# Kernel tuning notes

Hardware: AMD Instinct MI355X
Metric: run time of the kernel (lower is better)

## Reference

```python
import jax, jax.numpy as jnp
import numpy as np

L, D, H, DH, DF = 4, 512, 8, 64, 2048
B, S = 4, 2048
EPS = 1e-6  # fast-transformers causal-linear eps


def _ln(x, g, b, eps=1e-5):
    mu = jnp.mean(x, axis=-1, keepdims=True)
    var = jnp.var(x, axis=-1, keepdims=True)
    return (x - mu) * jax.lax.rsqrt(var + eps) * g + b


def _causal_linear(Q, K, V):
    # Q, K, V: [B, S, H, DH]; O(N) linear-attention recurrence over S
    Qs = jnp.moveaxis(Q, 1, 0)
    Ks = jnp.moveaxis(K, 1, 0)
    Vs = jnp.moveaxis(V, 1, 0)
    b = Q.shape[0]
    kv0 = jnp.zeros((b, H, DH, DH), Q.dtype)  # running sum of k v^T
    z0 = jnp.zeros((b, H, DH), Q.dtype)       # running sum of k

    def step(carry, qkv):
        kv, z = carry
        q, k, v = qkv  # each [B, H, DH]
        kv = kv + k[..., :, None] * v[..., None, :]
        z = z + k
        num = jnp.einsum('bhd,bhdm->bhm', q, kv)
        den = jnp.einsum('bhd,bhd->bh', q, z) + EPS
        return (kv, z), num / den[..., None]

    _, out = jax.lax.scan(step, (kv0, z0), (Qs, Ks, Vs))
    return jnp.moveaxis(out, 0, 1)  # [B, S, H, DH]


def _layer(x, p):
    Wq, bq, Wk, bk, Wv, bv, Wo, bo, W1, b1, W2, b2, g1, be1, g2, be2 = p
    b, s, _ = x.shape
    q = (x @ Wq + bq).reshape(b, s, H, DH)
    k = (x @ Wk + bk).reshape(b, s, H, DH)
    v = (x @ Wv + bv).reshape(b, s, H, DH)
    Qf = jax.nn.elu(q) + 1.0  # feature map phi(x) = elu(x) + 1
    Kf = jax.nn.elu(k) + 1.0
    a = _causal_linear(Qf, Kf, v).reshape(b, s, D)
    x = x + (a @ Wo + bo)            # residual (dropout=0)
    x = _ln(x, g1, be1)              # post-norm
    y = jax.nn.gelu(x @ W1 + b1, approximate=False) @ W2 + b2
    return _ln(x + y, g2, be2)


def _encoder(h, params, gf, bef):
    def body(x, p):
        return _layer(x, p), None
    x, _ = jax.lax.scan(body, h, params)
    return _ln(x, gf, bef)  # final LayerNorm from builder


def setup_inputs() -> dict:
    key = jax.random.key(0)
    ks = jax.random.split(key, 8)

    def w(k, shape, fan_in):
        return jax.random.normal(k, shape, jnp.float32) * (fan_in ** -0.5)

    return {
        'h': jax.random.normal(ks[0], (B, S, D), jnp.float32),
        'Wq': w(ks[1], (L, D, D), D), 'bq': jnp.zeros((L, D), jnp.float32),
        'Wk': w(ks[2], (L, D, D), D), 'bk': jnp.zeros((L, D), jnp.float32),
        'Wv': w(ks[3], (L, D, D), D), 'bv': jnp.zeros((L, D), jnp.float32),
        'Wo': w(ks[4], (L, D, D), D), 'bo': jnp.zeros((L, D), jnp.float32),
        'W1': w(ks[5], (L, D, DF), D), 'b1': jnp.zeros((L, DF), jnp.float32),
        'W2': w(ks[6], (L, DF, D), DF), 'b2': jnp.zeros((L, D), jnp.float32),
        'g1': jnp.ones((L, D), jnp.float32), 'be1': jnp.zeros((L, D), jnp.float32),
        'g2': jnp.ones((L, D), jnp.float32), 'be2': jnp.zeros((L, D), jnp.float32),
        'gf': jnp.ones((D,), jnp.float32), 'bef': jnp.zeros((D,), jnp.float32),
    }


def reference(h, Wq, bq, Wk, bk, Wv, bv, Wo, bo, W1, b1, W2, b2,
              g1, be1, g2, be2, gf, bef):
    params = (Wq, bq, Wk, bk, Wv, bv, Wo, bo, W1, b1, W2, b2, g1, be1, g2, be2)
    return _encoder(h, params, gf, bef)
```

## Files before the change

### kernel.cpp

```cpp
#include <hip/hip_runtime.h>
#include <hip/hip_bf16.h>
#include <math.h>

#define LAYERS 4
#define DMODEL 512
#define NH 8
#define DH 64
#define DFF 2048
#define NB 4
#define S_LEN 2048
#define MROWS 8192
#define CHUNK 64
#define NCHUNK 32
#define ATT_EPS 1e-6f
#define LN_EPS 1e-5f
#define SEGSTRIDE (MROWS * DMODEL)

typedef __attribute__((ext_vector_type(8))) short short8v;
typedef __attribute__((ext_vector_type(4))) float f32x4;

__device__ __forceinline__ float b2f(unsigned short u) {
    union { float f; unsigned u; } c; c.u = ((unsigned)u) << 16; return c.f;
}
__device__ __forceinline__ unsigned short f2b(float f) {
    union { float f; unsigned u; } c; c.f = f;
    unsigned r = c.u + 0x7FFFu + ((c.u >> 16) & 1u);
    return (unsigned short)(r >> 16);
}
__device__ __forceinline__ void gload16(const void* g, void* l) {
    __builtin_amdgcn_global_load_lds(
        (const __attribute__((address_space(1))) void*)g,
        (__attribute__((address_space(3))) void*)l, 16, 0, 0);
}
__device__ __forceinline__ float elu1f(float v) {
    return (v > 0.f) ? (v + 1.f) : __expf(v);
}
__device__ __forceinline__ float geluf(float v) {
    float u = 0.7978845608028654f * v * (1.f + 0.044715f * v * v);
    float th = 1.f - 2.f / (1.f + __expf(2.f * u));
    return 0.5f * v * (1.f + th);
}

template <int ACT, bool RESID, bool ATOMIC, bool WU, bool WBF16, int KSPLIT>
__global__ __launch_bounds__(512, 4) void gemm8(
    const unsigned short* __restrict__ A,
    const unsigned short* __restrict__ WT,
    const float* __restrict__ b0, const float* __restrict__ b1,
    const float* __restrict__ b2,
    const unsigned short* __restrict__ Xres,
    float* __restrict__ U, unsigned short* __restrict__ Cbf,
    int M, int N, int K)
{
    __shared__ short S[2][16384];

    const int t = threadIdx.x;
    const int m0 = blockIdx.x * 128, n0 = blockIdx.y * 128;
    const int kz = (KSPLIT > 1) ? blockIdx.z : 0;
    const int Kc = K / KSPLIT;
    const int kbeg = kz * Kc;
    const int lane = t & 63, wid = t >> 6;
    const int wm = (wid >> 2) * 64;
    const int wn = (wid & 3) * 32;
    const int fr = lane & 15, kg = lane >> 4;

    const unsigned short* gsrc[4];
    int ldso[4];
#pragma unroll
    for (int r = 0; r < 4; ++r) {
        const int u = (r & 1) ? (t + 512) : t;
        const bool isA = (r < 2);
        const int row = u >> 3, sp = u & 7, sl = sp ^ (row & 7);
        gsrc[r] = (isA ? A + (size_t)(m0 + row) * K
                       : WT + (size_t)(n0 + row) * K) + kbeg + sl * 8;
        ldso[r] = (isA ? 0 : 8192) + u * 8;
    }

    int aoff[2][4], boff[2][2];
#pragma unroll
    for (int h = 0; h < 2; ++h) {
#pragma unroll
        for (int m = 0; m < 4; ++m) {
            const int R = wm + m * 16 + fr;
            aoff[h][m] = R * 64 + (((h * 4 + kg) ^ (R & 7)) * 8);
        }
#pragma unroll
        for (int n = 0; n < 2; ++n) {
            const int R = wn + n * 16 + fr;
            boff[h][n] = 8192 + R * 64 + (((h * 4 + kg) ^ (R & 7)) * 8);
        }
    }

    f32x4 acc[4][2];
#pragma unroll
    for (int m = 0; m < 4; ++m)
#pragma unroll
        for (int n = 0; n < 2; ++n) acc[m][n] = (f32x4){0.f, 0.f, 0.f, 0.f};

#define STAGE(b, kt) do { _Pragma("unroll")                                  \
    for (int r = 0; r < 4; ++r)                                              \
        gload16(gsrc[r] + (size_t)(kt) * 64, &S[b][ldso[r]]); } while (0)

    const int NT = Kc >> 6;
    STAGE(0, 0);

    for (int td = 0; td < NT; ++td) {
        const int b = td & 1;
        if (td + 1 < NT) {
            STAGE(b ^ 1, td + 1);
            __builtin_amdgcn_sched_barrier(0);
            asm volatile("s_waitcnt vmcnt(4)");
        } else {
            __builtin_amdgcn_sched_barrier(0);
            asm volatile("s_waitcnt vmcnt(0)");
        }
        __builtin_amdgcn_sched_barrier(0);
        __builtin_amdgcn_s_barrier();
        __builtin_amdgcn_sched_barrier(0);

        short8v a0[4], b0f[2], a1[4], b1f[2];
#pragma unroll
        for (int m = 0; m < 4; ++m) a0[m] = *(const short8v*)&S[b][aoff[0][m]];
#pragma unroll
        for (int n = 0; n < 2; ++n) b0f[n] = *(const short8v*)&S[b][boff[0][n]];
#pragma unroll
        for (int m = 0; m < 4; ++m) a1[m] = *(const short8v*)&S[b][aoff[1][m]];
#pragma unroll
        for (int n = 0; n < 2; ++n) b1f[n] = *(const short8v*)&S[b][boff[1][n]];

        asm volatile("s_waitcnt lgkmcnt(6)");
        __builtin_amdgcn_sched_barrier(0);
        __builtin_amdgcn_s_setprio(1);
#pragma unroll
        for (int m = 0; m < 4; ++m)
#pragma unroll
            for (int n = 0; n < 2; ++n)
                acc[m][n] = __builtin_amdgcn_mfma_f32_16x16x32_bf16(
                    a0[m], b0f[n], acc[m][n], 0, 0, 0);
        __builtin_amdgcn_s_setprio(0);

        asm volatile("s_waitcnt lgkmcnt(0)");
        __builtin_amdgcn_sched_barrier(0);
        __builtin_amdgcn_s_setprio(1);
#pragma unroll
        for (int m = 0; m < 4; ++m)
#pragma unroll
            for (int n = 0; n < 2; ++n)
                acc[m][n] = __builtin_amdgcn_mfma_f32_16x16x32_bf16(
                    a1[m], b1f[n], acc[m][n], 0, 0, 0);
        __builtin_amdgcn_s_setprio(0);

        __builtin_amdgcn_sched_barrier(0);
        __builtin_amdgcn_s_barrier();
    }
#undef STAGE

    const int seg = (ACT == 3) ? (n0 >> 9) : 0;
    const float* bias = (ACT == 3) ? (seg == 0 ? b0 : (seg == 1 ? b1 : b2)) : b0;
    float bv[2];
#pragma unroll
    for (int n = 0; n < 2; ++n) {
        const int col = n0 + wn + n * 16 + fr;
        bv[n] = bias[(ACT == 3) ? (col - seg * 512) : col];
    }
    if (KSPLIT > 1 && kz != 0) { bv[0] = 0.f; bv[1] = 0.f; }

#pragma unroll
    for (int m = 0; m < 4; ++m)
#pragma unroll
        for (int n = 0; n < 2; ++n)
#pragma unroll
            for (int j = 0; j < 4; ++j) {
                const int row = m0 + wm + m * 16 + (lane >> 4) * 4 + j;
                const int col = n0 + wn + n * 16 + fr;
                float v = acc[m][n][j] + bv[n];
                if (RESID && kz == 0)
                    v += b2f(Xres[(size_t)row * 512 + col]);
                if (ACT == 1) v = elu1f(v);
                else if (ACT == 2) v = geluf(v);
                else if (ACT == 3) { if (seg < 2) v = elu1f(v); }
                if (ATOMIC) {
                    atomicAdd(&U[(size_t)row * N + col], v);
                } else if (WU) {
                    U[(size_t)row * N + col] = v;
                }
                if (WBF16) {
                    if (ACT == 3)
                        Cbf[(size_t)seg * SEGSTRIDE + (size_t)row * 512 + (col - seg * 512)] = f2b(v);
                    else
                        Cbf[(size_t)row * N + col] = f2b(v);
                }
            }
}

__global__ __launch_bounds__(256) void transpose_to_bf16(
    const float* __restrict__ W, unsigned short* __restrict__ WT, int K, int N)
{
    __shared__ float tile[32][33];
    const int k0 = blockIdx.x * 32, n0 = blockIdx.y * 32;
    const int tx = threadIdx.x & 31, ty = threadIdx.x >> 5;
#pragma unroll
    for (int i = ty; i < 32; i += 8)
        tile[i][tx] = W[(size_t)(k0 + i) * N + n0 + tx];
    __syncthreads();
#pragma unroll
    for (int i = ty; i < 32; i += 8)
        WT[(size_t)(n0 + i) * K + k0 + tx] = f2b(tile[tx][i]);
}

__global__ __launch_bounds__(256) void cvt_in(
    const float* __restrict__ h, unsigned short* __restrict__ xb, int n)
{
    const int i = (blockIdx.x * 256 + threadIdx.x) * 8;
    if (i >= n) return;
    f32x4 a = *(const f32x4*)(h + i);
    f32x4 b = *(const f32x4*)(h + i + 4);
    short8v p;
    p[0] = f2b(a[0]); p[1] = f2b(a[1]); p[2] = f2b(a[2]); p[3] = f2b(a[3]);
    p[4] = f2b(b[0]); p[5] = f2b(b[1]); p[6] = f2b(b[2]); p[7] = f2b(b[3]);
    *(short8v*)(xb + i) = p;
}

__device__ __forceinline__ int swzo(int row, int sl) {
    return row * 64 + ((sl ^ (row & 7)) << 3);
}

__global__ __launch_bounds__(256) void attn_stage1(
    const unsigned short* __restrict__ Kf, const unsigned short* __restrict__ Vf,
    unsigned short* __restrict__ KVp, float* __restrict__ zp)
{
    const int c = blockIdx.x, hh = blockIdx.y, bb = blockIdx.z;
    const int t = threadIdx.x;
    const int lane = t & 63, w = t >> 6;
    const int fr = lane & 15, g = lane >> 4;

    __shared__ unsigned short KTs[64 * 72];
    __shared__ unsigned short VTs[64 * 72];

    const size_t rowbase = (size_t)(bb * S_LEN + c * CHUNK);
    const int colbase = hh * DH;

    {
        const int r = lane, cs = w * 16;
        const unsigned short* kp = Kf + (rowbase + r) * DMODEL + colbase + cs;
        const unsigned short* vp = Vf + (rowbase + r) * DMODEL + colbase + cs;
        short8v k0 = *(const short8v*)kp, k1 = *(const short8v*)(kp + 8);
        short8v v0 = *(const short8v*)vp, v1 = *(const short8v*)(vp + 8);
#pragma unroll
        for (int i = 0; i < 8; ++i) {
            KTs[(cs + i) * 72 + r]     = (unsigned short)k0[i];
            KTs[(cs + 8 + i) * 72 + r] = (unsigned short)k1[i];
            VTs[(cs + i) * 72 + r]     = (unsigned short)v0[i];
            VTs[(cs + 8 + i) * 72 + r] = (unsigned short)v1[i];
        }
    }
    __syncthreads();

    f32x4 cacc[4];
#pragma unroll
    for (int nf = 0; nf < 4; ++nf) cacc[nf] = (f32x4){0.f, 0.f, 0.f, 0.f};

    const short8v a0 = *(const short8v*)&VTs[(w * 16 + fr) * 72 + g * 8];
    const short8v a1 = *(const short8v*)&VTs[(w * 16 + fr) * 72 + (4 + g) * 8];
#pragma unroll
    for (int nf = 0; nf < 4; ++nf) {
        short8v bq0 = *(const short8v*)&KTs[(nf * 16 + fr) * 72 + g * 8];
        short8v bq1 = *(const short8v*)&KTs[(nf * 16 + fr) * 72 + (4 + g) * 8];
        cacc[nf] = __builtin_amdgcn_mfma_f32_16x16x32_bf16(a0, bq0, cacc[nf], 0, 0, 0);
        cacc[nf] = __builtin_amdgcn_mfma_f32_16x16x32_bf16(a1, bq1, cacc[nf], 0, 0, 0);
    }

    const size_t base = ((size_t)(bb * NH + hh) * NCHUNK + c) * (DH * DH);
#pragma unroll
    for (int nf = 0; nf < 4; ++nf)
#pragma unroll
        for (int reg = 0; reg < 4; ++reg) {
            const int e = w * 16 + g * 4 + reg;
            const int d = nf * 16 + fr;
            KVp[base + e * 64 + d] = f2b(cacc[nf][reg]);
        }

    if (t < 64) {
        float s = 0.f;
#pragma unroll
        for (int sl = 0; sl < 8; ++sl) {
            short8v kv = *(const short8v*)&KTs[t * 72 + sl * 8];
#pragma unroll
            for (int i = 0; i < 8; ++i) s += b2f((unsigned short)kv[i]);
        }
        zp[((size_t)(bb * NH + hh) * NCHUNK + c) * DH + t] = s;
    }
}

__global__ __launch_bounds__(256) void attn_stage2(
    const unsigned short* __restrict__ KVp, unsigned short* __restrict__ KVb,
    float* __restrict__ zp)
{
    const int bh = blockIdx.x;
    const int e = blockIdx.y * 256 + threadIdx.x;
    const size_t base = (size_t)bh * NCHUNK * (DH * DH) + e;
    float run = 0.f;
#pragma unroll 4
    for (int c = 0; c < NCHUNK; ++c) {
        const float tmp = b2f(KVp[base + (size_t)c * (DH * DH)]);
        KVb[base + (size_t)c * (DH * DH)] = f2b(run);
        run += tmp;
    }
    if (blockIdx.y == 0 && threadIdx.x < DH) {
        float rz = 0.f;
        const size_t zb = (size_t)bh * NCHUNK * DH + threadIdx.x;
#pragma unroll 4
        for (int c = 0; c < NCHUNK; ++c) {
            const float tmp = zp[zb + c * DH];
            zp[zb + c * DH] = rz;
            rz += tmp;
        }
    }
}

__global__ __launch_bounds__(256) void attn_stage3(
    const unsigned short* __restrict__ Qf, const unsigned short* __restrict__ Kf,
    const unsigned short* __restrict__ Vf, const unsigned short* __restrict__ KVb,
    const float* __restrict__ zp, unsigned short* __restrict__ Af)
{
    const int c = blockIdx.x, hh = blockIdx.y, bb = blockIdx.z;
    const int t = threadIdx.x;
    const int lane = t & 63, w = t >> 6;
    const int fr = lane & 15, g = lane >> 4;

    __shared__ unsigned short Qs[4096];
    __shared__ unsigned short Ks[4096];
    __shared__ unsigned short KVts[4096];
    __shared__ unsigned short VTs[64 * 72];
    __shared__ unsigned short Ps[64 * 72];
    __shared__ float zsh[DH];
    __shared__ float den_lds[64];

    const size_t rowbase = (size_t)(bb * S_LEN + c * CHUNK);
    const int colbase = hh * DH;
    const size_t kvbase = ((size_t)(bb * NH + hh) * NCHUNK + c) * (DH * DH);

#pragma unroll
    for (int iss = 0; iss < 2; ++iss) {
        const int u = iss * 256 + t, row = u >> 3, sl = u & 7;
        const int ssl = (sl ^ (row & 7)) * 8;
        gload16(Qf + (rowbase + row) * DMODEL + colbase + ssl, &Qs[(size_t)u * 8]);
        gload16(Kf + (rowbase + row) * DMODEL + colbase + ssl, &Ks[(size_t)u * 8]);
        gload16(KVb + kvbase + row * 64 + ssl, &KVts[(size_t)u * 8]);
    }
    {
        const int r = lane, cs = w * 16;
        const unsigned short* vp = Vf + (rowbase + r) * DMODEL + colbase + cs;
        short8v v0 = *(const short8v*)vp, v1 = *(const short8v*)(vp + 8);
#pragma unroll
        for (int i = 0; i < 8; ++i) {
            VTs[(cs + i) * 72 + r]     = (unsigned short)v0[i];
            VTs[(cs + 8 + i) * 72 + r] = (unsigned short)v1[i];
        }
    }
    if (t < DH) zsh[t] = zp[((size_t)(bb * NH + hh) * NCHUNK + c) * DH + t];
    __syncthreads();

    f32x4 c1[4];
#pragma unroll
    for (int mf = 0; mf < 4; ++mf) c1[mf] = (f32x4){0.f, 0.f, 0.f, 0.f};
    {
        const short8v bq0 = *(const short8v*)&Qs[swzo(w * 16 + fr, g)];
        const short8v bq1 = *(const short8v*)&Qs[swzo(w * 16 + fr, 4 + g)];
#pragma unroll
        for (int mf = 0; mf < 4; ++mf) {
            short8v ak0 = *(const short8v*)&Ks[swzo(mf * 16 + fr, g)];
            short8v ak1 = *(const short8v*)&Ks[swzo(mf * 16 + fr, 4 + g)];
            c1[mf] = __builtin_amdgcn_mfma_f32_16x16x32_bf16(ak0, bq0, c1[mf], 0, 0, 0);
            c1[mf] = __builtin_amdgcn_mfma_f32_16x16x32_bf16(ak1, bq1, c1[mf], 0, 0, 0);
        }
    }

    const int i_my = w * 16 + fr;
    float dint = 0.f;
#pragma unroll
    for (int mf = 0; mf < 4; ++mf)
#pragma unroll
        for (int reg = 0; reg < 4; ++reg) {
            const int j = mf * 16 + g * 4 + reg;
            const float v = (j <= i_my) ? c1[mf][reg] : 0.f;
            dint += v;
            Ps[i_my * 72 + j] = f2b(v);
        }
    dint += __shfl_xor(dint, 16);
    dint += __shfl_xor(dint, 32);

    float dpre = 0.f;
#pragma unroll
    for (int sl = 0; sl < 8; ++sl) {
        short8v qv = *(const short8v*)&Qs[swzo(i_my, sl)];
#pragma unroll
        for (int e = 0; e < 8; ++e) dpre += b2f((unsigned short)qv[e]) * zsh[sl * 8 + e];
    }
    if (g == 0) den_lds[i_my] = dpre + dint + ATT_EPS;

    f32x4 acc[4];
#pragma unroll
    for (int nf = 0; nf < 4; ++nf) acc[nf] = (f32x4){0.f, 0.f, 0.f, 0.f};
    {
        const short8v aq0 = *(const short8v*)&Qs[swzo(w * 16 + fr, g)];
        const short8v aq1 = *(const short8v*)&Qs[swzo(w * 16 + fr, 4 + g)];
#pragma unroll
        for (int nf = 0; nf < 4; ++nf) {
            short8v bkv0 = *(const short8v*)&KVts[swzo(nf * 16 + fr, g)];
            short8v bkv1 = *(const short8v*)&KVts[swzo(nf * 16 + fr, 4 + g)];
            acc[nf] = __builtin_amdgcn_mfma_f32_16x16x32_bf16(aq0, bkv0, acc[nf], 0, 0, 0);
            acc[nf] = __builtin_amdgcn_mfma_f32_16x16x32_bf16(aq1, bkv1, acc[nf], 0, 0, 0);
        }
        const short8v ap0 = *(const short8v*)&Ps[(w * 16 + fr) * 72 + g * 8];
        const short8v ap1 = *(const short8v*)&Ps[(w * 16 + fr) * 72 + (4 + g) * 8];
#pragma unroll
        for (int nf = 0; nf < 4; ++nf) {
            short8v bv0 = *(const short8v*)&VTs[(nf * 16 + fr) * 72 + g * 8];
            short8v bv1 = *(const short8v*)&VTs[(nf * 16 + fr) * 72 + (4 + g) * 8];
            acc[nf] = __builtin_amdgcn_mfma_f32_16x16x32_bf16(ap0, bv0, acc[nf], 0, 0, 0);
            acc[nf] = __builtin_amdgcn_mfma_f32_16x16x32_bf16(ap1, bv1, acc[nf], 0, 0, 0);
        }
    }

#pragma unroll
    for (int reg = 0; reg < 4; ++reg) {
        const int i = w * 16 + g * 4 + reg;
        const float inv = 1.f / den_lds[i];
        unsigned short* dst = Af + (rowbase + i) * DMODEL + colbase;
#pragma unroll
        for (int nf = 0; nf < 4; ++nf)
            dst[nf * 16 + fr] = f2b(acc[nf][reg] * inv);
    }
}

__global__ __launch_bounds__(256) void ln_u2x(float* __restrict__ U,
                                              const float* __restrict__ g,
                                              const float* __restrict__ b,
                                              unsigned short* __restrict__ Xb,
                                              int ZERO)
{
    const size_t row = blockIdx.x * 4 + (threadIdx.x >> 6);
    const int t = threadIdx.x & 63;
    float* ur = U + row * DMODEL;
    f32x4 x0 = *(const f32x4*)&ur[t * 4];
    f32x4 x1 = *(const f32x4*)&ur[256 + t * 4];

    float s  = x0[0] + x0[1] + x0[2] + x0[3] + x1[0] + x1[1] + x1[2] + x1[3];
    float sq = x0[0]*x0[0] + x0[1]*x0[1] + x0[2]*x0[2] + x0[3]*x0[3] +
               x1[0]*x1[0] + x1[1]*x1[1] + x1[2]*x1[2] + x1[3]*x1[3];
#pragma unroll
    for (int m = 1; m < 64; m <<= 1) {
        s  += __shfl_xor(s, m);
        sq += __shfl_xor(sq, m);
    }
    const float mu  = s * (1.f / DMODEL);
    const float var = sq * (1.f / DMODEL) - mu * mu;
    const float rr  = rsqrtf(var + LN_EPS);

    const int c0 = t * 4, c1 = 256 + t * 4;
    f32x4 g0 = *(const f32x4*)&g[c0], g1v = *(const f32x4*)&g[c1];
    f32x4 b0 = *(const f32x4*)&b[c0], b1v = *(const f32x4*)&b[c1];
    unsigned short* xb = Xb + row * DMODEL;
    ushort4 u0, u1;
    u0.x = f2b((x0[0] - mu) * rr * g0[0] + b0[0]);
    u0.y = f2b((x0[1] - mu) * rr * g0[1] + b0[1]);
    u0.z = f2b((x0[2] - mu) * rr * g0[2] + b0[2]);
    u0.w = f2b((x0[3] - mu) * rr * g0[3] + b0[3]);
    u1.x = f2b((x1[0] - mu) * rr * g1v[0] + b1v[0]);
    u1.y = f2b((x1[1] - mu) * rr * g1v[1] + b1v[1]);
    u1.z = f2b((x1[2] - mu) * rr * g1v[2] + b1v[2]);
    u1.w = f2b((x1[3] - mu) * rr * g1v[3] + b1v[3]);
    *(ushort4*)&xb[c0] = u0;
    *(ushort4*)&xb[c1] = u1;
    if (ZERO) {
        *(f32x4*)&ur[c0] = (f32x4){0.f, 0.f, 0.f, 0.f};
        *(f32x4*)&ur[c1] = (f32x4){0.f, 0.f, 0.f, 0.f};
    }
}

__global__ __launch_bounds__(256) void ln_final(const unsigned short* __restrict__ Xb,
                                                const float* __restrict__ g,
                                                const float* __restrict__ b,
                                                float* __restrict__ Out)
{
    const size_t row = blockIdx.x * 4 + (threadIdx.x >> 6);
    const int t = threadIdx.x & 63;
    const unsigned short* xr = Xb + row * DMODEL;
    short8v xv = *(const short8v*)&xr[t * 8];
    float x[8];
#pragma unroll
    for (int i = 0; i < 8; ++i) x[i] = b2f((unsigned short)xv[i]);

    float s = 0.f, sq = 0.f;
#pragma unroll
    for (int i = 0; i < 8; ++i) { s += x[i]; sq += x[i] * x[i]; }
#pragma unroll
    for (int m = 1; m < 64; m <<= 1) {
        s  += __shfl_xor(s, m);
        sq += __shfl_xor(sq, m);
    }
    const float mu  = s * (1.f / DMODEL);
    const float var = sq * (1.f / DMODEL) - mu * mu;
    const float rr  = rsqrtf(var + LN_EPS);

    float* orow = Out + row * DMODEL + t * 8;
    f32x4 o0, o1;
#pragma unroll
    for (int i = 0; i < 4; ++i) {
        o0[i] = (x[i] - mu) * rr * g[t * 8 + i] + b[t * 8 + i];
        o1[i] = (x[4 + i] - mu) * rr * g[t * 8 + 4 + i] + b[t * 8 + 4 + i];
    }
    *(f32x4*)orow = o0;
    *(f32x4*)(orow + 4) = o1;
}

extern "C" void kernel_launch(void* const* d_in, const int* in_sizes, int n_in,
                              void* d_out, int out_size, void* d_ws, size_t ws_size,
                              hipStream_t stream)
{
    const float* h   = (const float*)d_in[0];
    const float* Wq  = (const float*)d_in[1];
    const float* bq  = (const float*)d_in[2];
    const float* Wk  = (const float*)d_in[3];
    const float* bk  = (const float*)d_in[4];
    const float* Wv  = (const float*)d_in[5];
    const float* bv  = (const float*)d_in[6];
    const float* Wo  = (const float*)d_in[7];
    const float* bo  = (const float*)d_in[8];
    const float* W1  = (const float*)d_in[9];
    const float* b1  = (const float*)d_in[10];
    const float* W2  = (const float*)d_in[11];
    const float* b2  = (const float*)d_in[12];
    const float* g1  = (const float*)d_in[13];
    const float* be1 = (const float*)d_in[14];
    const float* g2  = (const float*)d_in[15];
    const float* be2 = (const float*)d_in[16];
    const float* gf  = (const float*)d_in[17];
    const float* bef = (const float*)d_in[18];

    char* ws = (char*)d_ws;
    const size_t MB = 1024 * 1024;
    unsigned short* x_bf = (unsigned short*)(ws);
    unsigned short* qkv  = (unsigned short*)(ws + 8 * MB);
    unsigned short* qb   = qkv;
    unsigned short* kb   = qkv + SEGSTRIDE;
    unsigned short* vb   = qkv + 2 * (size_t)SEGSTRIDE;
    unsigned short* ab   = (unsigned short*)(ws + 32 * MB);
    unsigned short* hid  = (unsigned short*)(ws + 8 * MB);
    unsigned short* KVp  = (unsigned short*)(ws + 40 * MB);
    unsigned short* KVb  = (unsigned short*)(ws + 48 * MB);
    float* U             = (float*)(ws + 40 * MB);
    float* zp            = (float*)(ws + 56 * MB);
    unsigned short* WTall = (unsigned short*)(ws + 57 * MB);

    const int M = MROWS, D = DMODEL, DF = DFF;
    const size_t LSTR = 3 * 1024 * 1024;

    cvt_in<<<dim3(M * D / (256 * 8)), 256, 0, stream>>>(h, x_bf, M * D);
    for (int l = 0; l < LAYERS; ++l) {
        unsigned short* WL = WTall + (size_t)l * LSTR;
        transpose_to_bf16<<<dim3(D / 32, D / 32), 256, 0, stream>>>(Wq + (size_t)l * D * D, WL, D, D);
        transpose_to_bf16<<<dim3(D / 32, D / 32), 256, 0, stream>>>(Wk + (size_t)l * D * D, WL + 262144, D, D);
        transpose_to_bf16<<<dim3(D / 32, D / 32), 256, 0, stream>>>(Wv + (size_t)l * D * D, WL + 524288, D, D);
        transpose_to_bf16<<<dim3(D / 32, D / 32), 256, 0, stream>>>(Wo + (size_t)l * D * D, WL + 786432, D, D);
        transpose_to_bf16<<<dim3(D / 32, DF / 32), 256, 0, stream>>>(W1 + (size_t)l * D * DF, WL + 1048576, D, DF);
        transpose_to_bf16<<<dim3(DF / 32, D / 32), 256, 0, stream>>>(W2 + (size_t)l * DF * D, WL + 2097152, DF, D);
    }

    for (int l = 0; l < LAYERS; ++l) {
        unsigned short* WL = WTall + (size_t)l * LSTR;
        const unsigned short* WqkvT = WL;
        const unsigned short* WoT   = WL + 786432;
        const unsigned short* W1T   = WL + 1048576;
        const unsigned short* W2T   = WL + 2097152;

        gemm8<3, false, false, false, true, 1>
            <<<dim3(M / 128, 1536 / 128), 512, 0, stream>>>(
            x_bf, WqkvT, bq + (size_t)l * D, bk + (size_t)l * D, bv + (size_t)l * D,
            nullptr, nullptr, qkv, M, 1536, D);

        attn_stage1<<<dim3(NCHUNK, NH, NB), 256, 0, stream>>>(kb, vb, KVp, zp);
        attn_stage2<<<dim3(NB * NH, 16), 256, 0, stream>>>(KVp, KVb, zp);
        attn_stage3<<<dim3(NCHUNK, NH, NB), 256, 0, stream>>>(qb, kb, vb, KVb, zp, ab);

        gemm8<0, true, false, true, false, 1>
            <<<dim3(M / 128, D / 128), 512, 0, stream>>>(
            ab, WoT, bo + (size_t)l * D, nullptr, nullptr, x_bf, U, nullptr, M, D, D);
        ln_u2x<<<dim3(M / 4), 256, 0, stream>>>(U, g1 + (size_t)l * D, be1 + (size_t)l * D, x_bf, 1);

        gemm8<2, false, false, false, true, 1>
            <<<dim3(M / 128, DF / 128), 512, 0, stream>>>(
            x_bf, W1T, b1 + (size_t)l * DF, nullptr, nullptr, nullptr, nullptr, hid, M, DF, D);
        gemm8<0, true, true, false, false, 2>
            <<<dim3(M / 128, D / 128, 2), 512, 0, stream>>>(
            hid, W2T, b2 + (size_t)l * D, nullptr, nullptr, x_bf, U, nullptr, M, D, DF);
        ln_u2x<<<dim3(M / 4), 256, 0, stream>>>(U, g2 + (size_t)l * D, be2 + (size_t)l * D, x_bf, 0);
    }

    ln_final<<<dim3(M / 4), 256, 0, stream>>>(x_bf, gf, bef, (float*)d_out);
}
```

Before: 637.3 us.

## Add wider 128x256-tile GEMM for QKV and FFN1, batch weight transposes

Adds a gemmw kernel with 128x256 output tiles (each wave computes 64x64 with 4x4 MFMA accumulators) and a K-step of 32, used for the QKV projection and the first FFN GEMM. The wider N tile reuses each A tile over more columns, cutting A-operand global and LDS traffic per FLOP. The trade is more accumulator registers per thread and fewer blocks in the grid. It also merges the per-layer weight transpose launches into six launches using a z-dimension over layers, and strips the unused QKV path from gemm8.

```diff
diff --git a/kernel.cpp b/kernel.cpp
--- a/kernel.cpp
+++ b/kernel.cpp
@@ -41,12 +41,135 @@
     return 0.5f * v * (1.f + th);
 }
 
+template <int ACT>
+__global__ __launch_bounds__(512, 6) void gemmw(
+    const unsigned short* __restrict__ A,
+    const unsigned short* __restrict__ WT,
+    const float* __restrict__ b0, const float* __restrict__ b1,
+    const float* __restrict__ b2,
+    unsigned short* __restrict__ Cbf,
+    int M, int N, int K)
+{
+    __shared__ short S[2][12288];
+
+    const int t = threadIdx.x;
+    const int m0 = blockIdx.x * 128, n0 = blockIdx.y * 256;
+    const int lane = t & 63, wid = t >> 6;
+    const int wm = (wid >> 2) * 64;
+    const int wn = (wid & 3) * 64;
+    const int fr = lane & 15, kg = lane >> 4;
+
+    const unsigned short* gA;
+    const unsigned short* gB0;
+    const unsigned short* gB1;
+    int loA, loB0, loB1;
+    {
+        const int rowA = t >> 2, spA = t & 3;
+        gA = A + (size_t)(m0 + rowA) * K + (spA ^ ((rowA >> 1) & 3)) * 8;
+        loA = t * 8;
+        const int rB0 = t >> 2, sB0 = t & 3;
+        gB0 = WT + (size_t)(n0 + rB0) * K + (sB0 ^ ((rB0 >> 1) & 3)) * 8;
+        loB0 = 4096 + t * 8;
+        const int u1 = t + 512;
+        const int rB1 = u1 >> 2, sB1 = u1 & 3;
+        gB1 = WT + (size_t)(n0 + rB1) * K + (sB1 ^ ((rB1 >> 1) & 3)) * 8;
+        loB1 = 4096 + u1 * 8;
+    }
+
+    int aoff[4], boff[4];
+#pragma unroll
+    for (int m = 0; m < 4; ++m) {
+        const int R = wm + m * 16 + fr;
+        aoff[m] = R * 32 + ((kg ^ ((R >> 1) & 3)) << 3);
+    }
+#pragma unroll
+    for (int n = 0; n < 4; ++n) {
+        const int R = wn + n * 16 + fr;
+        boff[n] = 4096 + R * 32 + ((kg ^ ((R >> 1) & 3)) << 3);
+    }
+
+    f32x4 acc[4][4];
+#pragma unroll
+    for (int m = 0; m < 4; ++m)
+#pragma unroll
+        for (int n = 0; n < 4; ++n) acc[m][n] = (f32x4){0.f, 0.f, 0.f, 0.f};
+
+#define STAGE(b, kt) do {                                       \
+    gload16(gA + (size_t)(kt) * 32, &S[b][loA]);                \
+    gload16(gB0 + (size_t)(kt) * 32, &S[b][loB0]);              \
+    gload16(gB1 + (size_t)(kt) * 32, &S[b][loB1]); } while (0)
+
+    const int NT = K >> 5;
+    STAGE(0, 0);
+
+    for (int td = 0; td < NT; ++td) {
+        const int b = td & 1;
+        if (td + 1 < NT) {
+            STAGE(b ^ 1, td + 1);
+            __builtin_amdgcn_sched_barrier(0);
+            asm volatile("s_waitcnt vmcnt(3)");
+        } else {
+            __builtin_amdgcn_sched_barrier(0);
+            asm volatile("s_waitcnt vmcnt(0)");
+        }
+        __builtin_amdgcn_sched_barrier(0);
+        __builtin_amdgcn_s_barrier();
+        __builtin_amdgcn_sched_barrier(0);
+
+        short8v af[4], bf[4];
+#pragma unroll
+        for (int m = 0; m < 4; ++m) af[m] = *(const short8v*)&S[b][aoff[m]];
+#pragma unroll
+        for (int n = 0; n < 4; ++n) bf[n] = *(const short8v*)&S[b][boff[n]];
+
+        asm volatile("s_waitcnt lgkmcnt(0)");
+        __builtin_amdgcn_sched_barrier(0);
+        __builtin_amdgcn_s_setprio(1);
+#pragma unroll
+        for (int m = 0; m < 4; ++m)
+#pragma unroll
+            for (int n = 0; n < 4; ++n)
+                acc[m][n] = __builtin_amdgcn_mfma_f32_16x16x32_bf16(
+                    af[m], bf[n], acc[m][n], 0, 0, 0);
+        __builtin_amdgcn_s_setprio(0);
+
+        __builtin_amdgcn_sched_barrier(0);
+        __builtin_amdgcn_s_barrier();
+    }
+#undef STAGE
+
+    const int seg = (ACT == 3) ? (n0 >> 9) : 0;
+    const float* bias = (ACT == 3) ? (seg == 0 ? b0 : (seg == 1 ? b1 : b2)) : b0;
+    float bv[4];
+#pragma unroll
+    for (int n = 0; n < 4; ++n) {
+        const int col = n0 + wn + n * 16 + fr;
+        bv[n] = bias[(ACT == 3) ? (col - seg * 512) : col];
+    }
+
+#pragma unroll
+    for (int m = 0; m < 4; ++m)
+#pragma unroll
+        for (int n = 0; n < 4; ++n)
+#pragma unroll
+            for (int j = 0; j < 4; ++j) {
+                const int row = m0 + wm + m * 16 + (lane >> 4) * 4 + j;
+                const int col = n0 + wn + n * 16 + fr;
+                float v = acc[m][n][j] + bv[n];
+                if (ACT == 2) v = geluf(v);
+                else if (ACT == 3) { if (seg < 2) v = elu1f(v); }
+                if (ACT == 3)
+                    Cbf[(size_t)seg * SEGSTRIDE + (size_t)row * 512 + (col - seg * 512)] = f2b(v);
+                else
+                    Cbf[(size_t)row * N + col] = f2b(v);
+            }
+}
+
 template <int ACT, bool RESID, bool ATOMIC, bool WU, bool WBF16, int KSPLIT>
 __global__ __launch_bounds__(512, 4) void gemm8(
     const unsigned short* __restrict__ A,
     const unsigned short* __restrict__ WT,
-    const float* __restrict__ b0, const float* __restrict__ b1,
-    const float* __restrict__ b2,
+    const float* __restrict__ b0,
     const unsigned short* __restrict__ Xres,
     float* __restrict__ U, unsigned short* __restrict__ Cbf,
     int M, int N, int K)
@@ -154,14 +277,10 @@
     }
 #undef STAGE
 
-    const int seg = (ACT == 3) ? (n0 >> 9) : 0;
-    const float* bias = (ACT == 3) ? (seg == 0 ? b0 : (seg == 1 ? b1 : b2)) : b0;
     float bv[2];
 #pragma unroll
-    for (int n = 0; n < 2; ++n) {
-        const int col = n0 + wn + n * 16 + fr;
-        bv[n] = bias[(ACT == 3) ? (col - seg * 512) : col];
-    }
+    for (int n = 0; n < 2; ++n)
+        bv[n] = b0[n0 + wn + n * 16 + fr];
     if (KSPLIT > 1 && kz != 0) { bv[0] = 0.f; bv[1] = 0.f; }
 
 #pragma unroll
@@ -177,25 +296,24 @@
                     v += b2f(Xres[(size_t)row * 512 + col]);
                 if (ACT == 1) v = elu1f(v);
                 else if (ACT == 2) v = geluf(v);
-                else if (ACT == 3) { if (seg < 2) v = elu1f(v); }
                 if (ATOMIC) {
                     atomicAdd(&U[(size_t)row * N + col], v);
                 } else if (WU) {
                     U[(size_t)row * N + col] = v;
                 }
-                if (WBF16) {
-                    if (ACT == 3)
-                        Cbf[(size_t)seg * SEGSTRIDE + (size_t)row * 512 + (col - seg * 512)] = f2b(v);
-                    else
-                        Cbf[(size_t)row * N + col] = f2b(v);
-                }
+                if (WBF16)
+                    Cbf[(size_t)row * N + col] = f2b(v);
             }
 }
 
 __global__ __launch_bounds__(256) void transpose_to_bf16(
-    const float* __restrict__ W, unsigned short* __restrict__ WT, int K, int N)
+    const float* __restrict__ W, unsigned short* __restrict__ WT, int K, int N,
+    size_t wstride, size_t tstride)
 {
     __shared__ float tile[32][33];
+    const int l = blockIdx.z;
+    W += (size_t)l * wstride;
+    WT += (size_t)l * tstride;
     const int k0 = blockIdx.x * 32, n0 = blockIdx.y * 32;
     const int tx = threadIdx.x & 31, ty = threadIdx.x >> 5;
 #pragma unroll
@@ -557,15 +675,18 @@
     const size_t LSTR = 3 * 1024 * 1024;
 
     cvt_in<<<dim3(M * D / (256 * 8)), 256, 0, stream>>>(h, x_bf, M * D);
-    for (int l = 0; l < LAYERS; ++l) {
-        unsigned short* WL = WTall + (size_t)l * LSTR;
-        transpose_to_bf16<<<dim3(D / 32, D / 32), 256, 0, stream>>>(Wq + (size_t)l * D * D, WL, D, D);
-        transpose_to_bf16<<<dim3(D / 32, D / 32), 256, 0, stream>>>(Wk + (size_t)l * D * D, WL + 262144, D, D);
-        transpose_to_bf16<<<dim3(D / 32, D / 32), 256, 0, stream>>>(Wv + (size_t)l * D * D, WL + 524288, D, D);
-        transpose_to_bf16<<<dim3(D / 32, D / 32), 256, 0, stream>>>(Wo + (size_t)l * D * D, WL + 786432, D, D);
-        transpose_to_bf16<<<dim3(D / 32, DF / 32), 256, 0, stream>>>(W1 + (size_t)l * D * DF, WL + 1048576, D, DF);
-        transpose_to_bf16<<<dim3(DF / 32, D / 32), 256, 0, stream>>>(W2 + (size_t)l * DF * D, WL + 2097152, DF, D);
-    }
+    transpose_to_bf16<<<dim3(D / 32, D / 32, LAYERS), 256, 0, stream>>>(
+        Wq, WTall, D, D, (size_t)D * D, LSTR);
+    transpose_to_bf16<<<dim3(D / 32, D / 32, LAYERS), 256, 0, stream>>>(
+        Wk, WTall + 262144, D, D, (size_t)D * D, LSTR);
+    transpose_to_bf16<<<dim3(D / 32, D / 32, LAYERS), 256, 0, stream>>>(
+        Wv, WTall + 524288, D, D, (size_t)D * D, LSTR);
+    transpose_to_bf16<<<dim3(D / 32, D / 32, LAYERS), 256, 0, stream>>>(
+        Wo, WTall + 786432, D, D, (size_t)D * D, LSTR);
+    transpose_to_bf16<<<dim3(D / 32, DF / 32, LAYERS), 256, 0, stream>>>(
+        W1, WTall + 1048576, D, DF, (size_t)D * DF, LSTR);
+    transpose_to_bf16<<<dim3(DF / 32, D / 32, LAYERS), 256, 0, stream>>>(
+        W2, WTall + 2097152, DF, D, (size_t)DF * D, LSTR);
 
     for (int l = 0; l < LAYERS; ++l) {
         unsigned short* WL = WTall + (size_t)l * LSTR;
@@ -574,10 +695,9 @@
         const unsigned short* W1T   = WL + 1048576;
         const unsigned short* W2T   = WL + 2097152;
 
-        gemm8<3, false, false, false, true, 1>
-            <<<dim3(M / 128, 1536 / 128), 512, 0, stream>>>(
+        gemmw<3><<<dim3(M / 128, 1536 / 256), 512, 0, stream>>>(
             x_bf, WqkvT, bq + (size_t)l * D, bk + (size_t)l * D, bv + (size_t)l * D,
-            nullptr, nullptr, qkv, M, 1536, D);
+            qkv, M, 1536, D);
 
         attn_stage1<<<dim3(NCHUNK, NH, NB), 256, 0, stream>>>(kb, vb, KVp, zp);
         attn_stage2<<<dim3(NB * NH, 16), 256, 0, stream>>>(KVp, KVb, zp);
@@ -585,15 +705,14 @@
 
         gemm8<0, true, false, true, false, 1>
             <<<dim3(M / 128, D / 128), 512, 0, stream>>>(
-            ab, WoT, bo + (size_t)l * D, nullptr, nullptr, x_bf, U, nullptr, M, D, D);
+            ab, WoT, bo + (size_t)l * D, x_bf, U, nullptr, M, D, D);
         ln_u2x<<<dim3(M / 4), 256, 0, stream>>>(U, g1 + (size_t)l * D, be1 + (size_t)l * D, x_bf, 1);
 
-        gemm8<2, false, false, false, true, 1>
-            <<<dim3(M / 128, DF / 128), 512, 0, stream>>>(
-            x_bf, W1T, b1 + (size_t)l * DF, nullptr, nullptr, nullptr, nullptr, hid, M, DF, D);
+        gemmw<2><<<dim3(M / 128, DF / 256), 512, 0, stream>>>(
+            x_bf, W1T, b1 + (size_t)l * DF, nullptr, nullptr, hid, M, DF, D);
         gemm8<0, true, true, false, false, 2>
             <<<dim3(M / 128, D / 128, 2), 512, 0, stream>>>(
-            hid, W2T, b2 + (size_t)l * D, nullptr, nullptr, x_bf, U, nullptr, M, D, DF);
+            hid, W2T, b2 + (size_t)l * D, x_bf, U, nullptr, M, D, DF);
         ln_u2x<<<dim3(M / 4), 256, 0, stream>>>(U, g2 + (size_t)l * D, be2 + (size_t)l * D, x_bf, 0);
     }
 
```

Measured after the change: 1.533 ms. +140.5%, slower.
